# Performance work log

Measured on AMD Instinct MI355X. Metric: run time of the kernel, lower is better.

Reference implementation:

```python
import jax, jax.numpy as jnp
import numpy as np

D_TOK = 64
HID = 128


def _init_linear(key, fan_in, fan_out, bias_fill=None):
    kw, kb = jax.random.split(key)
    bound = 1.0 / np.sqrt(fan_in)
    W = jax.random.uniform(kw, (fan_in, fan_out), jnp.float32, -bound, bound)
    if bias_fill is None:
        b = jax.random.uniform(kb, (fan_out,), jnp.float32, -bound, bound)
    else:
        b = jnp.full((fan_out,), bias_fill, jnp.float32)
    return W, b


def setup_inputs() -> dict:
    key = jax.random.key(0)
    ks = jax.random.split(key, 7)
    N, E = 20000, 16
    tokens = jax.random.normal(ks[0], (N, E, D_TOK), jnp.float32)
    enc_W1, enc_b1 = _init_linear(ks[1], D_TOK, HID)
    enc_W2, enc_b2 = _init_linear(ks[2], HID, HID)
    spec_W1, spec_b1 = _init_linear(ks[3], 4 * HID, HID)
    spec_W2, spec_b2 = _init_linear(ks[4], HID, 1)
    def_W1, def_b1 = _init_linear(ks[5], 3 * HID, HID)
    def_W2, def_b2 = _init_linear(ks[6], HID, 1, bias_fill=-1.0)  # config.defer_bias
    return {
        "tokens": tokens,
        "enc_W1": enc_W1, "enc_b1": enc_b1, "enc_W2": enc_W2, "enc_b2": enc_b2,
        "spec_W1": spec_W1, "spec_b1": spec_b1, "spec_W2": spec_W2, "spec_b2": spec_b2,
        "def_W1": def_W1, "def_b1": def_b1, "def_W2": def_W2, "def_b2": def_b2,
        "full_index": 0,
        "top_k": 2,
    }


def _apply_top_k_mask(logits, full_index, top_k):
    # logits: [N, E]; mimic torch _apply_top_k_mask
    N, E = logits.shape
    if E <= 1:
        return logits
    neg = jnp.finfo(logits.dtype).min
    k = max(1, min(int(top_k), E - 1))
    masked = logits.at[:, full_index].set(neg)
    _, idx = jax.lax.top_k(masked, k)  # [N, k]
    rows = jnp.arange(N)[:, None]
    keep = jnp.zeros((N, E), bool).at[rows, idx].set(True)
    keep = keep.at[:, full_index].set(False)
    return jnp.where(keep, masked, neg)


def reference(tokens, enc_W1, enc_b1, enc_W2, enc_b2,
              spec_W1, spec_b1, spec_W2, spec_b2,
              def_W1, def_b1, def_W2, def_b2,
              full_index, top_k):
    neg = jnp.finfo(tokens.dtype).min
    # token encoder: two Linear+ReLU, applied per (row, expert)
    h = jax.nn.relu(tokens @ enc_W1 + enc_b1)
    encoded = jax.nn.relu(h @ enc_W2 + enc_b2)          # [N, E, H]
    full_token = encoded[:, full_index:full_index + 1]  # [N, 1, H]
    global_token = encoded.mean(axis=1, keepdims=True)  # [N, 1, H]
    token_delta = encoded - full_token
    global_delta = encoded - global_token
    pair = jnp.concatenate([encoded, token_delta, global_delta,
                            jnp.abs(token_delta)], axis=-1)  # [N, E, 4H]
    spec_h = jax.nn.relu(pair @ spec_W1 + spec_b1)
    specialist_logits = (spec_h @ spec_W2 + spec_b2)[..., 0]  # [N, E]
    specialist_logits = specialist_logits.at[:, full_index].set(neg)
    sparse_logits = _apply_top_k_mask(specialist_logits, full_index, top_k)
    w = jax.nn.softmax(sparse_logits, axis=1)
    w = w.at[:, full_index].set(0.0)
    mass = w.sum(axis=1, keepdims=True)
    w = jnp.where(mass > 0, w / jnp.maximum(mass, 1e-8), jnp.zeros_like(w))
    pooled = jnp.concatenate([full_token[:, 0], global_token[:, 0],
                              jnp.abs(token_delta).mean(axis=1)], axis=1)  # [N, 3H]
    def_h = jax.nn.relu(pooled @ def_W1 + def_b1)
    defer_prob = jax.nn.sigmoid(def_h @ def_W2 + def_b2)  # [N, 1]
    return w, defer_prob
```

## Files before the change

### kernel.cpp

```cpp
#include <hip/hip_runtime.h>
#include <math.h>

#define E 16
#define D 64
#define H 128
#define R 4
#define ROWS (R * E)
#define MW 16

__global__ void wabc_prep(const float* __restrict__ specW1, float* __restrict__ wabc) {
    int i = blockIdx.x * blockDim.x + threadIdx.x;
    if (i < H * H) {
        wabc[i] = specW1[i] + specW1[H * H + i] + specW1[2 * H * H + i];
    }
}

__device__ inline float waveReduceSum(float v) {
#pragma unroll
    for (int off = 32; off; off >>= 1) v += __shfl_xor(v, off, 64);
    return v;
}

template <bool USE_WABC>
__global__ __launch_bounds__(256, 2)
void router_kernel(const float* __restrict__ tokens,
                   const float* __restrict__ encW1, const float* __restrict__ encB1,
                   const float* __restrict__ encW2, const float* __restrict__ encB2,
                   const float* __restrict__ specW1, const float* __restrict__ specB1,
                   const float* __restrict__ specW2,
                   const float* __restrict__ defW1, const float* __restrict__ defB1,
                   const float* __restrict__ defW2, const float* __restrict__ defB2,
                   const int* __restrict__ fiPtr, const int* __restrict__ tkPtr,
                   const float* __restrict__ wabc,
                   float* __restrict__ out, int N) {
    __shared__ float bufA[ROWS * H];
    __shared__ float bufB[ROWS * H];
    __shared__ float s_glob[R * H];
    __shared__ float s_mabs[R * H];
    __shared__ float s_bias[R * H];
    __shared__ float s_pB[2 * R * H];
    __shared__ float s_pD[2 * R * H];
    __shared__ float s_logits[ROWS];
    __shared__ float s_dred[R];

    const int tid   = threadIdx.x;
    const int n0    = blockIdx.x * R;
    const int fi    = fiPtr[0];
    const int lane  = tid & 63;
    const int wq    = tid >> 6;
    const int j0    = lane * 2;
    const int mbase = wq * MW;

    {
        const size_t base  = (size_t)n0 * (E * D);
        const size_t total = (size_t)N * (E * D);
        float4* dst = (float4*)bufA;
#pragma unroll
        for (int it = 0; it < 4; it++) {
            int f = tid + it * 256;
            size_t off = base + (size_t)f * 4;
            float4 v = make_float4(0.f, 0.f, 0.f, 0.f);
            if (off + 3 < total) v = *(const float4*)(tokens + off);
            dst[f] = v;
        }
    }
    __syncthreads();

    {
        float acc[MW][2];
#pragma unroll
        for (int m = 0; m < MW; m++) { acc[m][0] = 0.f; acc[m][1] = 0.f; }
#pragma unroll 2
        for (int k = 0; k < D; k += 4) {
            float2 w0 = *(const float2*)(encW1 + (k + 0) * H + j0);
            float2 w1 = *(const float2*)(encW1 + (k + 1) * H + j0);
            float2 w2 = *(const float2*)(encW1 + (k + 2) * H + j0);
            float2 w3 = *(const float2*)(encW1 + (k + 3) * H + j0);
#pragma unroll
            for (int m = 0; m < MW; m++) {
                float4 t = *(const float4*)(bufA + (mbase + m) * D + k);
                acc[m][0] = fmaf(t.w, w3.x, fmaf(t.z, w2.x, fmaf(t.y, w1.x, fmaf(t.x, w0.x, acc[m][0]))));
                acc[m][1] = fmaf(t.w, w3.y, fmaf(t.z, w2.y, fmaf(t.y, w1.y, fmaf(t.x, w0.y, acc[m][1]))));
            }
        }
        float2 b = *(const float2*)(encB1 + j0);
#pragma unroll
        for (int m = 0; m < MW; m++) {
            float2 o;
            o.x = fmaxf(acc[m][0] + b.x, 0.f);
            o.y = fmaxf(acc[m][1] + b.y, 0.f);
            *(float2*)(bufB + (mbase + m) * H + j0) = o;
        }
    }
    __syncthreads();

    {
        float acc[MW][2];
#pragma unroll
        for (int m = 0; m < MW; m++) { acc[m][0] = 0.f; acc[m][1] = 0.f; }
#pragma unroll 2
        for (int k = 0; k < H; k += 4) {
            float2 w0 = *(const float2*)(encW2 + (k + 0) * H + j0);
            float2 w1 = *(const float2*)(encW2 + (k + 1) * H + j0);
            float2 w2 = *(const float2*)(encW2 + (k + 2) * H + j0);
            float2 w3 = *(const float2*)(encW2 + (k + 3) * H + j0);
#pragma unroll
            for (int m = 0; m < MW; m++) {
                float4 t = *(const float4*)(bufB + (mbase + m) * H + k);
                acc[m][0] = fmaf(t.w, w3.x, fmaf(t.z, w2.x, fmaf(t.y, w1.x, fmaf(t.x, w0.x, acc[m][0]))));
                acc[m][1] = fmaf(t.w, w3.y, fmaf(t.z, w2.y, fmaf(t.y, w1.y, fmaf(t.x, w0.y, acc[m][1]))));
            }
        }
        float2 b = *(const float2*)(encB2 + j0);
#pragma unroll
        for (int m = 0; m < MW; m++) {
            float2 o;
            o.x = fmaxf(acc[m][0] + b.x, 0.f);
            o.y = fmaxf(acc[m][1] + b.y, 0.f);
            *(float2*)(bufA + (mbase + m) * H + j0) = o;
        }
    }
    __syncthreads();

    {
        const int r4 = tid >> 6;
        const int cb = tid & 63;
#pragma unroll
        for (int half = 0; half < 2; half++) {
            const int c = cb + half * 64;
            const float* er = bufA + (r4 * E) * H + c;
            float s = 0.f;
#pragma unroll
            for (int e = 0; e < E; e++) s += er[e * H];
            float g  = s * (1.f / 16.f);
            float fc = er[fi * H];
            float ma = 0.f;
#pragma unroll
            for (int e = 0; e < E; e++) {
                float d = er[e * H] - fc;
                float a = fabsf(d);
                bufB[(r4 * E + e) * H + c] = a;
                ma += a;
            }
            s_glob[r4 * H + c] = g;
            s_mabs[r4 * H + c] = ma * (1.f / 16.f);
        }
    }
    __syncthreads();

    {
        const int jp = tid & 63;
        const int jj = jp * 2;
        const int kh = (tid >> 6) & 1;
        const int rg = tid >> 7;
        const int c0 = kh * 64;
        const float* Wb = specW1 + H * H;
        const float* Wc = specW1 + 2 * H * H;
        float accB[2][2] = {{0.f, 0.f}, {0.f, 0.f}};
        float accD[2][2] = {{0.f, 0.f}, {0.f, 0.f}};
        for (int cc = 0; cc < 64; cc++) {
            const int c = c0 + cc;
            float2 wb = *(const float2*)(Wb + c * H + jj);
            float2 wc = *(const float2*)(Wc + c * H + jj);
            float2 d0 = *(const float2*)(defW1 + c * H + jj);
            float2 d1 = *(const float2*)(defW1 + (H + c) * H + jj);
            float2 d2 = *(const float2*)(defW1 + (2 * H + c) * H + jj);
#pragma unroll
            for (int rl = 0; rl < 2; rl++) {
                const int r = rg * 2 + rl;
                float fv = bufA[(r * E + fi) * H + c];
                float gv = s_glob[r * H + c];
                float mv = s_mabs[r * H + c];
                accB[rl][0] = fmaf(fv, wb.x, accB[rl][0]);
                accB[rl][1] = fmaf(fv, wb.y, accB[rl][1]);
                accB[rl][0] = fmaf(gv, wc.x, accB[rl][0]);
                accB[rl][1] = fmaf(gv, wc.y, accB[rl][1]);
                accD[rl][0] = fmaf(fv, d0.x, accD[rl][0]);
                accD[rl][1] = fmaf(fv, d0.y, accD[rl][1]);
                accD[rl][0] = fmaf(gv, d1.x, accD[rl][0]);
                accD[rl][1] = fmaf(gv, d1.y, accD[rl][1]);
                accD[rl][0] = fmaf(mv, d2.x, accD[rl][0]);
                accD[rl][1] = fmaf(mv, d2.y, accD[rl][1]);
            }
        }
#pragma unroll
        for (int rl = 0; rl < 2; rl++) {
            const int r = rg * 2 + rl;
            *(float2*)(s_pB + (kh * R + r) * H + jj) = make_float2(accB[rl][0], accB[rl][1]);
            *(float2*)(s_pD + (kh * R + r) * H + jj) = make_float2(accD[rl][0], accD[rl][1]);
        }
    }
    __syncthreads();

    {
        float dv = 0.f;
#pragma unroll
        for (int t = 0; t < 2; t++) {
            const int j = lane + t * 64;
            float pb = s_pB[wq * H + j] + s_pB[(R + wq) * H + j];
            s_bias[wq * H + j] = specB1[j] - pb;
            float pd = defB1[j] + s_pD[wq * H + j] + s_pD[(R + wq) * H + j];
            dv += fmaxf(pd, 0.f) * defW2[j];
        }
        dv = waveReduceSum(dv);
        if (lane == 0) s_dred[wq] = dv;
    }
    __syncthreads();

    {
        float acc[MW][2];
#pragma unroll
        for (int m = 0; m < MW; m++) { acc[m][0] = 0.f; acc[m][1] = 0.f; }
        for (int c = 0; c < H; c += 4) {
            float2 wa0, wa1, wa2, wa3;
            if (USE_WABC) {
                wa0 = *(const float2*)(wabc + (c + 0) * H + j0);
                wa1 = *(const float2*)(wabc + (c + 1) * H + j0);
                wa2 = *(const float2*)(wabc + (c + 2) * H + j0);
                wa3 = *(const float2*)(wabc + (c + 3) * H + j0);
            } else {
#pragma unroll
                for (int t = 0; t < 4; t++) {
                    float2 a0 = *(const float2*)(specW1 + (c + t) * H + j0);
                    float2 a1 = *(const float2*)(specW1 + (H + c + t) * H + j0);
                    float2 a2 = *(const float2*)(specW1 + (2 * H + c + t) * H + j0);
                    float2 s2; s2.x = a0.x + a1.x + a2.x; s2.y = a0.y + a1.y + a2.y;
                    if (t == 0) wa0 = s2; else if (t == 1) wa1 = s2; else if (t == 2) wa2 = s2; else wa3 = s2;
                }
            }
            float2 wd0 = *(const float2*)(specW1 + (3 * H + c + 0) * H + j0);
            float2 wd1 = *(const float2*)(specW1 + (3 * H + c + 1) * H + j0);
            float2 wd2 = *(const float2*)(specW1 + (3 * H + c + 2) * H + j0);
            float2 wd3 = *(const float2*)(specW1 + (3 * H + c + 3) * H + j0);
#pragma unroll
            for (int m = 0; m < MW; m++) {
                float4 ev = *(const float4*)(bufA + (mbase + m) * H + c);
                float4 av = *(const float4*)(bufB + (mbase + m) * H + c);
                float a0 = acc[m][0], a1 = acc[m][1];
                a0 = fmaf(ev.x, wa0.x, a0); a0 = fmaf(ev.y, wa1.x, a0);
                a0 = fmaf(ev.z, wa2.x, a0); a0 = fmaf(ev.w, wa3.x, a0);
                a0 = fmaf(av.x, wd0.x, a0); a0 = fmaf(av.y, wd1.x, a0);
                a0 = fmaf(av.z, wd2.x, a0); a0 = fmaf(av.w, wd3.x, a0);
                a1 = fmaf(ev.x, wa0.y, a1); a1 = fmaf(ev.y, wa1.y, a1);
                a1 = fmaf(ev.z, wa2.y, a1); a1 = fmaf(ev.w, wa3.y, a1);
                a1 = fmaf(av.x, wd0.y, a1); a1 = fmaf(av.y, wd1.y, a1);
                a1 = fmaf(av.z, wd2.y, a1); a1 = fmaf(av.w, wd3.y, a1);
                acc[m][0] = a0; acc[m][1] = a1;
            }
        }
        float2 bn = *(const float2*)(s_bias + wq * H + j0);
        float2 w2 = *(const float2*)(specW2 + j0);
#pragma unroll
        for (int m = 0; m < MW; m++) {
            float h0 = fmaxf(acc[m][0] + bn.x, 0.f);
            float h1 = fmaxf(acc[m][1] + bn.y, 0.f);
            float p  = h0 * w2.x + h1 * w2.y;
            p = waveReduceSum(p);
            if (lane == 0) s_logits[mbase + m] = p;
        }
    }
    __syncthreads();

    if (tid < R && (n0 + tid) < N) {
        const int r = tid;
        const int n = n0 + r;
        float s = s_dred[r] + defB2[0];
        out[(size_t)N * E + n] = 1.f / (1.f + expf(-s));
        int k = tkPtr[0];
        if (k < 1) k = 1;
        if (k > E - 1) k = E - 1;
        unsigned chosen = 0u;
        for (int kk = 0; kk < k; kk++) {
            float bv = -INFINITY;
            int bi = 0;
            for (int e = 0; e < E; e++) {
                if (e == fi || ((chosen >> e) & 1u)) continue;
                float v = s_logits[r * E + e];
                if (v > bv) { bv = v; bi = e; }
            }
            chosen |= (1u << bi);
        }
        float mx = -INFINITY;
        for (int e = 0; e < E; e++)
            if ((chosen >> e) & 1u) { float v = s_logits[r * E + e]; if (v > mx) mx = v; }
        float ssum = 0.f;
        for (int e = 0; e < E; e++)
            if ((chosen >> e) & 1u) ssum += expf(s_logits[r * E + e] - mx);
        float inv = 1.f / ssum;
        for (int e = 0; e < E; e++) {
            float wv = 0.f;
            if ((chosen >> e) & 1u) wv = expf(s_logits[r * E + e] - mx) * inv;
            out[(size_t)n * E + e] = wv;
        }
    }
}

extern "C" void kernel_launch(void* const* d_in, const int* in_sizes, int n_in,
                              void* d_out, int out_size, void* d_ws, size_t ws_size,
                              hipStream_t stream) {
    (void)n_in; (void)out_size;
    const float* tokens = (const float*)d_in[0];
    const float* encW1  = (const float*)d_in[1];
    const float* encB1  = (const float*)d_in[2];
    const float* encW2  = (const float*)d_in[3];
    const float* encB2  = (const float*)d_in[4];
    const float* specW1 = (const float*)d_in[5];
    const float* specB1 = (const float*)d_in[6];
    const float* specW2 = (const float*)d_in[7];
    const float* defW1  = (const float*)d_in[9];
    const float* defB1  = (const float*)d_in[10];
    const float* defW2  = (const float*)d_in[11];
    const float* defB2  = (const float*)d_in[12];
    const int*   fiPtr  = (const int*)d_in[13];
    const int*   tkPtr  = (const int*)d_in[14];
    float* out = (float*)d_out;

    const int N = in_sizes[0] / (E * D);
    const int grid = (N + R - 1) / R;
    const bool useWs = (d_ws != nullptr) && (ws_size >= (size_t)(H * H * sizeof(float)));

    if (useWs) {
        wabc_prep<<<(H * H + 255) / 256, 256, 0, stream>>>(specW1, (float*)d_ws);
        router_kernel<true><<<grid, 256, 0, stream>>>(
            tokens, encW1, encB1, encW2, encB2, specW1, specB1, specW2,
            defW1, defB1, defW2, defB2, fiPtr, tkPtr, (const float*)d_ws, out, N);
    } else {
        router_kernel<false><<<grid, 256, 0, stream>>>(
            tokens, encW1, encB1, encW2, encB2, specW1, specB1, specW2,
            defW1, defB1, defW2, defB2, fiPtr, tkPtr, nullptr, out, N);
    }
}
```

Measured before the change: 761.2 us.

## Remap GEMMs so each lane owns a token row and waves own output-column slices

Restructures all three per-token GEMMs so each lane computes one (row, expert) token and each wave computes a 32-column slice. Weights are read as wave-uniform (scalar) loads and tokens are read straight from global memory, with no LDS staging. The |token_delta| buffer is no longer stored; it is recomputed on the fly from the encoded values and the full token, and LDS rows are padded to avoid bank conflicts. Specialist logits become per-wave partial sums that are added in the final top-k stage. This removes the cross-lane wave reductions, but each thread now holds 32 accumulators, and the uncoalesced per-row token loads may hurt.

```diff
diff --git a/kernel.cpp b/kernel.cpp
--- a/kernel.cpp
+++ b/kernel.cpp
@@ -6,19 +6,13 @@
 #define H 128
 #define R 4
 #define ROWS (R * E)
-#define MW 16
+#define PAD 130
 
 __global__ void wabc_prep(const float* __restrict__ specW1, float* __restrict__ wabc) {
     int i = blockIdx.x * blockDim.x + threadIdx.x;
     if (i < H * H) {
         wabc[i] = specW1[i] + specW1[H * H + i] + specW1[2 * H * H + i];
     }
-}
-
-__device__ inline float waveReduceSum(float v) {
-#pragma unroll
-    for (int off = 32; off; off >>= 1) v += __shfl_xor(v, off, 64);
-    return v;
 }
 
 template <bool USE_WABC>
@@ -33,129 +27,111 @@
                    const int* __restrict__ fiPtr, const int* __restrict__ tkPtr,
                    const float* __restrict__ wabc,
                    float* __restrict__ out, int N) {
-    __shared__ float bufA[ROWS * H];
-    __shared__ float bufB[ROWS * H];
+    __shared__ float bufH[ROWS * PAD];
+    __shared__ float bufE[ROWS * PAD];
+    __shared__ float s_full[R * H];
     __shared__ float s_glob[R * H];
     __shared__ float s_mabs[R * H];
     __shared__ float s_bias[R * H];
-    __shared__ float s_pB[2 * R * H];
-    __shared__ float s_pD[2 * R * H];
-    __shared__ float s_logits[ROWS];
+    __shared__ float s_lp[4 * ROWS];
     __shared__ float s_dred[R];
 
-    const int tid   = threadIdx.x;
-    const int n0    = blockIdx.x * R;
-    const int fi    = fiPtr[0];
-    const int lane  = tid & 63;
-    const int wq    = tid >> 6;
-    const int j0    = lane * 2;
-    const int mbase = wq * MW;
-
-    {
-        const size_t base  = (size_t)n0 * (E * D);
-        const size_t total = (size_t)N * (E * D);
-        float4* dst = (float4*)bufA;
-#pragma unroll
-        for (int it = 0; it < 4; it++) {
-            int f = tid + it * 256;
-            size_t off = base + (size_t)f * 4;
-            float4 v = make_float4(0.f, 0.f, 0.f, 0.f);
-            if (off + 3 < total) v = *(const float4*)(tokens + off);
-            dst[f] = v;
-        }
-    }
-    __syncthreads();
-
-    {
-        float acc[MW][2];
-#pragma unroll
-        for (int m = 0; m < MW; m++) { acc[m][0] = 0.f; acc[m][1] = 0.f; }
-#pragma unroll 2
-        for (int k = 0; k < D; k += 4) {
-            float2 w0 = *(const float2*)(encW1 + (k + 0) * H + j0);
-            float2 w1 = *(const float2*)(encW1 + (k + 1) * H + j0);
-            float2 w2 = *(const float2*)(encW1 + (k + 2) * H + j0);
-            float2 w3 = *(const float2*)(encW1 + (k + 3) * H + j0);
-#pragma unroll
-            for (int m = 0; m < MW; m++) {
-                float4 t = *(const float4*)(bufA + (mbase + m) * D + k);
-                acc[m][0] = fmaf(t.w, w3.x, fmaf(t.z, w2.x, fmaf(t.y, w1.x, fmaf(t.x, w0.x, acc[m][0]))));
-                acc[m][1] = fmaf(t.w, w3.y, fmaf(t.z, w2.y, fmaf(t.y, w1.y, fmaf(t.x, w0.y, acc[m][1]))));
-            }
-        }
-        float2 b = *(const float2*)(encB1 + j0);
-#pragma unroll
-        for (int m = 0; m < MW; m++) {
+    const int tid  = threadIdx.x;
+    const int lane = tid & 63;
+    const int wq   = tid >> 6;
+    const int jb   = __builtin_amdgcn_readfirstlane(wq) * 32;
+    const int n0   = blockIdx.x * R;
+    const int fi   = fiPtr[0];
+    const int l    = lane;
+
+    int tokRow = n0 * E + l;
+    if (tokRow >= N * E) tokRow = 0;
+    const float* tokRowPtr = tokens + (size_t)tokRow * D;
+
+    float acc[32];
+
+#pragma unroll
+    for (int j = 0; j < 32; j++) acc[j] = 0.f;
+    for (int k = 0; k < D; k += 2) {
+        float2 a2 = *(const float2*)(tokRowPtr + k);
+        const float* __restrict__ w0 = encW1 + k * H + jb;
+        const float* __restrict__ w1 = encW1 + (k + 1) * H + jb;
+#pragma unroll
+        for (int j = 0; j < 32; j++) {
+            acc[j] = fmaf(a2.x, w0[j], acc[j]);
+            acc[j] = fmaf(a2.y, w1[j], acc[j]);
+        }
+    }
+    {
+        const float* __restrict__ b = encB1 + jb;
+#pragma unroll
+        for (int t = 0; t < 16; t++) {
             float2 o;
-            o.x = fmaxf(acc[m][0] + b.x, 0.f);
-            o.y = fmaxf(acc[m][1] + b.y, 0.f);
-            *(float2*)(bufB + (mbase + m) * H + j0) = o;
-        }
-    }
-    __syncthreads();
-
-    {
-        float acc[MW][2];
-#pragma unroll
-        for (int m = 0; m < MW; m++) { acc[m][0] = 0.f; acc[m][1] = 0.f; }
-#pragma unroll 2
-        for (int k = 0; k < H; k += 4) {
-            float2 w0 = *(const float2*)(encW2 + (k + 0) * H + j0);
-            float2 w1 = *(const float2*)(encW2 + (k + 1) * H + j0);
-            float2 w2 = *(const float2*)(encW2 + (k + 2) * H + j0);
-            float2 w3 = *(const float2*)(encW2 + (k + 3) * H + j0);
-#pragma unroll
-            for (int m = 0; m < MW; m++) {
-                float4 t = *(const float4*)(bufB + (mbase + m) * H + k);
-                acc[m][0] = fmaf(t.w, w3.x, fmaf(t.z, w2.x, fmaf(t.y, w1.x, fmaf(t.x, w0.x, acc[m][0]))));
-                acc[m][1] = fmaf(t.w, w3.y, fmaf(t.z, w2.y, fmaf(t.y, w1.y, fmaf(t.x, w0.y, acc[m][1]))));
-            }
-        }
-        float2 b = *(const float2*)(encB2 + j0);
-#pragma unroll
-        for (int m = 0; m < MW; m++) {
+            o.x = fmaxf(acc[2 * t] + b[2 * t], 0.f);
+            o.y = fmaxf(acc[2 * t + 1] + b[2 * t + 1], 0.f);
+            *(float2*)(bufH + l * PAD + jb + 2 * t) = o;
+        }
+    }
+    __syncthreads();
+
+#pragma unroll
+    for (int j = 0; j < 32; j++) acc[j] = 0.f;
+    for (int k = 0; k < H; k += 2) {
+        float2 a2 = *(const float2*)(bufH + l * PAD + k);
+        const float* __restrict__ w0 = encW2 + k * H + jb;
+        const float* __restrict__ w1 = encW2 + (k + 1) * H + jb;
+#pragma unroll
+        for (int j = 0; j < 32; j++) {
+            acc[j] = fmaf(a2.x, w0[j], acc[j]);
+            acc[j] = fmaf(a2.y, w1[j], acc[j]);
+        }
+    }
+    {
+        const float* __restrict__ b = encB2 + jb;
+#pragma unroll
+        for (int t = 0; t < 16; t++) {
             float2 o;
-            o.x = fmaxf(acc[m][0] + b.x, 0.f);
-            o.y = fmaxf(acc[m][1] + b.y, 0.f);
-            *(float2*)(bufA + (mbase + m) * H + j0) = o;
-        }
-    }
-    __syncthreads();
-
-    {
-        const int r4 = tid >> 6;
+            o.x = fmaxf(acc[2 * t] + b[2 * t], 0.f);
+            o.y = fmaxf(acc[2 * t + 1] + b[2 * t + 1], 0.f);
+            *(float2*)(bufE + l * PAD + jb + 2 * t) = o;
+        }
+    }
+    __syncthreads();
+
+    {
+        const int r  = tid >> 6;
         const int cb = tid & 63;
 #pragma unroll
         for (int half = 0; half < 2; half++) {
             const int c = cb + half * 64;
-            const float* er = bufA + (r4 * E) * H + c;
+            const float* er = bufE + (r * E) * PAD + c;
+            float v[E];
+#pragma unroll
+            for (int e = 0; e < E; e++) v[e] = er[e * PAD];
             float s = 0.f;
 #pragma unroll
-            for (int e = 0; e < E; e++) s += er[e * H];
-            float g  = s * (1.f / 16.f);
-            float fc = er[fi * H];
+            for (int e = 0; e < E; e++) s += v[e];
+            float fc = v[fi];
             float ma = 0.f;
 #pragma unroll
-            for (int e = 0; e < E; e++) {
-                float d = er[e * H] - fc;
-                float a = fabsf(d);
-                bufB[(r4 * E + e) * H + c] = a;
-                ma += a;
-            }
-            s_glob[r4 * H + c] = g;
-            s_mabs[r4 * H + c] = ma * (1.f / 16.f);
-        }
-    }
-    __syncthreads();
-
+            for (int e = 0; e < E; e++) ma += fabsf(v[e] - fc);
+            s_full[r * H + c] = fc;
+            s_glob[r * H + c] = s * (1.f / 16.f);
+            s_mabs[r * H + c] = ma * (1.f / 16.f);
+        }
+    }
+    __syncthreads();
+
+    float* s_pB = bufH;
+    float* s_pD = bufH + 2 * R * H;
     {
         const int jp = tid & 63;
         const int jj = jp * 2;
         const int kh = (tid >> 6) & 1;
         const int rg = tid >> 7;
         const int c0 = kh * 64;
-        const float* Wb = specW1 + H * H;
-        const float* Wc = specW1 + 2 * H * H;
+        const float* __restrict__ Wb = specW1 + H * H;
+        const float* __restrict__ Wc = specW1 + 2 * H * H;
         float accB[2][2] = {{0.f, 0.f}, {0.f, 0.f}};
         float accD[2][2] = {{0.f, 0.f}, {0.f, 0.f}};
         for (int cc = 0; cc < 64; cc++) {
@@ -168,7 +144,7 @@
 #pragma unroll
             for (int rl = 0; rl < 2; rl++) {
                 const int r = rg * 2 + rl;
-                float fv = bufA[(r * E + fi) * H + c];
+                float fv = s_full[r * H + c];
                 float gv = s_glob[r * H + c];
                 float mv = s_mabs[r * H + c];
                 accB[rl][0] = fmaf(fv, wb.x, accB[rl][0]);
@@ -202,62 +178,56 @@
             float pd = defB1[j] + s_pD[wq * H + j] + s_pD[(R + wq) * H + j];
             dv += fmaxf(pd, 0.f) * defW2[j];
         }
-        dv = waveReduceSum(dv);
+#pragma unroll
+        for (int off = 32; off; off >>= 1) dv += __shfl_xor(dv, off, 64);
         if (lane == 0) s_dred[wq] = dv;
     }
     __syncthreads();
 
-    {
-        float acc[MW][2];
-#pragma unroll
-        for (int m = 0; m < MW; m++) { acc[m][0] = 0.f; acc[m][1] = 0.f; }
-        for (int c = 0; c < H; c += 4) {
-            float2 wa0, wa1, wa2, wa3;
+#pragma unroll
+    for (int j = 0; j < 32; j++) acc[j] = 0.f;
+    {
+        const int rr = l >> 4;
+        const float* __restrict__ Wd = specW1 + 3 * H * H;
+        for (int k = 0; k < H; k += 2) {
+            float2 e2 = *(const float2*)(bufE + l * PAD + k);
+            float2 f2 = *(const float2*)(s_full + rr * H + k);
+            float a0 = fabsf(e2.x - f2.x);
+            float a1 = fabsf(e2.y - f2.y);
+            const float* __restrict__ wd0 = Wd + k * H + jb;
+            const float* __restrict__ wd1 = Wd + (k + 1) * H + jb;
             if (USE_WABC) {
-                wa0 = *(const float2*)(wabc + (c + 0) * H + j0);
-                wa1 = *(const float2*)(wabc + (c + 1) * H + j0);
-                wa2 = *(const float2*)(wabc + (c + 2) * H + j0);
-                wa3 = *(const float2*)(wabc + (c + 3) * H + j0);
+                const float* __restrict__ wa0 = wabc + k * H + jb;
+                const float* __restrict__ wa1 = wabc + (k + 1) * H + jb;
+#pragma unroll
+                for (int j = 0; j < 32; j++) {
+                    acc[j] = fmaf(e2.x, wa0[j], acc[j]);
+                    acc[j] = fmaf(e2.y, wa1[j], acc[j]);
+                    acc[j] = fmaf(a0, wd0[j], acc[j]);
+                    acc[j] = fmaf(a1, wd1[j], acc[j]);
+                }
             } else {
-#pragma unroll
-                for (int t = 0; t < 4; t++) {
-                    float2 a0 = *(const float2*)(specW1 + (c + t) * H + j0);
-                    float2 a1 = *(const float2*)(specW1 + (H + c + t) * H + j0);
-                    float2 a2 = *(const float2*)(specW1 + (2 * H + c + t) * H + j0);
-                    float2 s2; s2.x = a0.x + a1.x + a2.x; s2.y = a0.y + a1.y + a2.y;
-                    if (t == 0) wa0 = s2; else if (t == 1) wa1 = s2; else if (t == 2) wa2 = s2; else wa3 = s2;
+                const float* __restrict__ p0 = specW1 + k * H + jb;
+                const float* __restrict__ p1 = specW1 + (k + 1) * H + jb;
+#pragma unroll
+                for (int j = 0; j < 32; j++) {
+                    float w_a0 = p0[j] + p0[H * H + j] + p0[2 * H * H + j];
+                    float w_a1 = p1[j] + p1[H * H + j] + p1[2 * H * H + j];
+                    acc[j] = fmaf(e2.x, w_a0, acc[j]);
+                    acc[j] = fmaf(e2.y, w_a1, acc[j]);
+                    acc[j] = fmaf(a0, wd0[j], acc[j]);
+                    acc[j] = fmaf(a1, wd1[j], acc[j]);
                 }
             }
-            float2 wd0 = *(const float2*)(specW1 + (3 * H + c + 0) * H + j0);
-            float2 wd1 = *(const float2*)(specW1 + (3 * H + c + 1) * H + j0);
-            float2 wd2 = *(const float2*)(specW1 + (3 * H + c + 2) * H + j0);
-            float2 wd3 = *(const float2*)(specW1 + (3 * H + c + 3) * H + j0);
-#pragma unroll
-            for (int m = 0; m < MW; m++) {
-                float4 ev = *(const float4*)(bufA + (mbase + m) * H + c);
-                float4 av = *(const float4*)(bufB + (mbase + m) * H + c);
-                float a0 = acc[m][0], a1 = acc[m][1];
-                a0 = fmaf(ev.x, wa0.x, a0); a0 = fmaf(ev.y, wa1.x, a0);
-                a0 = fmaf(ev.z, wa2.x, a0); a0 = fmaf(ev.w, wa3.x, a0);
-                a0 = fmaf(av.x, wd0.x, a0); a0 = fmaf(av.y, wd1.x, a0);
-                a0 = fmaf(av.z, wd2.x, a0); a0 = fmaf(av.w, wd3.x, a0);
-                a1 = fmaf(ev.x, wa0.y, a1); a1 = fmaf(ev.y, wa1.y, a1);
-                a1 = fmaf(ev.z, wa2.y, a1); a1 = fmaf(ev.w, wa3.y, a1);
-                a1 = fmaf(av.x, wd0.y, a1); a1 = fmaf(av.y, wd1.y, a1);
-                a1 = fmaf(av.z, wd2.y, a1); a1 = fmaf(av.w, wd3.y, a1);
-                acc[m][0] = a0; acc[m][1] = a1;
-            }
-        }
-        float2 bn = *(const float2*)(s_bias + wq * H + j0);
-        float2 w2 = *(const float2*)(specW2 + j0);
-#pragma unroll
-        for (int m = 0; m < MW; m++) {
-            float h0 = fmaxf(acc[m][0] + bn.x, 0.f);
-            float h1 = fmaxf(acc[m][1] + bn.y, 0.f);
-            float p  = h0 * w2.x + h1 * w2.y;
-            p = waveReduceSum(p);
-            if (lane == 0) s_logits[mbase + m] = p;
-        }
+        }
+        float p = 0.f;
+        const float* __restrict__ w2 = specW2 + jb;
+#pragma unroll
+        for (int j = 0; j < 32; j++) {
+            float b = s_bias[rr * H + jb + j];
+            p += fmaxf(acc[j] + b, 0.f) * w2[j];
+        }
+        s_lp[wq * ROWS + l] = p;
     }
     __syncthreads();
 
@@ -266,6 +236,11 @@
         const int n = n0 + r;
         float s = s_dred[r] + defB2[0];
         out[(size_t)N * E + n] = 1.f / (1.f + expf(-s));
+        float lg[E];
+#pragma unroll
+        for (int e = 0; e < E; e++)
+            lg[e] = s_lp[0 * ROWS + r * E + e] + s_lp[1 * ROWS + r * E + e]
+                  + s_lp[2 * ROWS + r * E + e] + s_lp[3 * ROWS + r * E + e];
         int k = tkPtr[0];
         if (k < 1) k = 1;
         if (k > E - 1) k = E - 1;
@@ -275,21 +250,21 @@
             int bi = 0;
             for (int e = 0; e < E; e++) {
                 if (e == fi || ((chosen >> e) & 1u)) continue;
-                float v = s_logits[r * E + e];
+                float v = lg[e];
                 if (v > bv) { bv = v; bi = e; }
             }
             chosen |= (1u << bi);
         }
         float mx = -INFINITY;
         for (int e = 0; e < E; e++)
-            if ((chosen >> e) & 1u) { float v = s_logits[r * E + e]; if (v > mx) mx = v; }
+            if ((chosen >> e) & 1u) { float v = lg[e]; if (v > mx) mx = v; }
         float ssum = 0.f;
         for (int e = 0; e < E; e++)
-            if ((chosen >> e) & 1u) ssum += expf(s_logits[r * E + e] - mx);
+            if ((chosen >> e) & 1u) ssum += expf(lg[e] - mx);
         float inv = 1.f / ssum;
         for (int e = 0; e < E; e++) {
             float wv = 0.f;
-            if ((chosen >> e) & 1u) wv = expf(s_logits[r * E + e] - mx) * inv;
+            if ((chosen >> e) & 1u) wv = expf(lg[e] - mx) * inv;
             out[(size_t)n * E + e] = wv;
         }
     }
```

Result: slower. 943.3 us (+23.9%).

## Retile GEMMs to 8x4 register tiles and recompute abs-delta on the fly

Applied to the files above, without the earlier changes.

Each wave's GEMM stages switch from 16 rows by 2 columns per lane to 8 rows by 4 columns, split across two half-waves. This halves the LDS activation reads per FMA and uses float4 weight loads. The abs(token_delta) tensor is no longer written to shared memory; it is recomputed from the encoded values and a new per-row full-token buffer inside the specialist GEMM. The freed buffer is reused for the partial sums, which lowers LDS footprint. The logits reduction now runs over 32-lane half-waves, and register pressure changes with the larger column tile.

```diff
diff --git a/kernel.cpp b/kernel.cpp
--- a/kernel.cpp
+++ b/kernel.cpp
@@ -13,12 +13,6 @@
     if (i < H * H) {
         wabc[i] = specW1[i] + specW1[H * H + i] + specW1[2 * H * H + i];
     }
-}
-
-__device__ inline float waveReduceSum(float v) {
-#pragma unroll
-    for (int off = 32; off; off >>= 1) v += __shfl_xor(v, off, 64);
-    return v;
 }
 
 template <bool USE_WABC>
@@ -35,11 +29,10 @@
                    float* __restrict__ out, int N) {
     __shared__ float bufA[ROWS * H];
     __shared__ float bufB[ROWS * H];
+    __shared__ float s_full[R * H];
     __shared__ float s_glob[R * H];
     __shared__ float s_mabs[R * H];
     __shared__ float s_bias[R * H];
-    __shared__ float s_pB[2 * R * H];
-    __shared__ float s_pD[2 * R * H];
     __shared__ float s_logits[ROWS];
     __shared__ float s_dred[R];
 
@@ -48,8 +41,11 @@
     const int fi    = fiPtr[0];
     const int lane  = tid & 63;
     const int wq    = tid >> 6;
-    const int j0    = lane * 2;
     const int mbase = wq * MW;
+    const int hw    = lane >> 5;
+    const int jl    = lane & 31;
+    const int jw0   = jl * 4;
+    const int mb2   = mbase + hw * 8;
 
     {
         const size_t base  = (size_t)n0 * (E * D);
@@ -67,57 +63,69 @@
     __syncthreads();
 
     {
-        float acc[MW][2];
-#pragma unroll
-        for (int m = 0; m < MW; m++) { acc[m][0] = 0.f; acc[m][1] = 0.f; }
+        float acc[8][4];
+#pragma unroll
+        for (int m = 0; m < 8; m++)
+#pragma unroll
+            for (int j = 0; j < 4; j++) acc[m][j] = 0.f;
 #pragma unroll 2
         for (int k = 0; k < D; k += 4) {
-            float2 w0 = *(const float2*)(encW1 + (k + 0) * H + j0);
-            float2 w1 = *(const float2*)(encW1 + (k + 1) * H + j0);
-            float2 w2 = *(const float2*)(encW1 + (k + 2) * H + j0);
-            float2 w3 = *(const float2*)(encW1 + (k + 3) * H + j0);
-#pragma unroll
-            for (int m = 0; m < MW; m++) {
-                float4 t = *(const float4*)(bufA + (mbase + m) * D + k);
+            float4 w0 = *(const float4*)(encW1 + (k + 0) * H + jw0);
+            float4 w1 = *(const float4*)(encW1 + (k + 1) * H + jw0);
+            float4 w2 = *(const float4*)(encW1 + (k + 2) * H + jw0);
+            float4 w3 = *(const float4*)(encW1 + (k + 3) * H + jw0);
+#pragma unroll
+            for (int m = 0; m < 8; m++) {
+                float4 t = *(const float4*)(bufA + (mb2 + m) * D + k);
                 acc[m][0] = fmaf(t.w, w3.x, fmaf(t.z, w2.x, fmaf(t.y, w1.x, fmaf(t.x, w0.x, acc[m][0]))));
                 acc[m][1] = fmaf(t.w, w3.y, fmaf(t.z, w2.y, fmaf(t.y, w1.y, fmaf(t.x, w0.y, acc[m][1]))));
-            }
-        }
-        float2 b = *(const float2*)(encB1 + j0);
-#pragma unroll
-        for (int m = 0; m < MW; m++) {
-            float2 o;
+                acc[m][2] = fmaf(t.w, w3.z, fmaf(t.z, w2.z, fmaf(t.y, w1.z, fmaf(t.x, w0.z, acc[m][2]))));
+                acc[m][3] = fmaf(t.w, w3.w, fmaf(t.z, w2.w, fmaf(t.y, w1.w, fmaf(t.x, w0.w, acc[m][3]))));
+            }
+        }
+        float4 b = *(const float4*)(encB1 + jw0);
+#pragma unroll
+        for (int m = 0; m < 8; m++) {
+            float4 o;
             o.x = fmaxf(acc[m][0] + b.x, 0.f);
             o.y = fmaxf(acc[m][1] + b.y, 0.f);
-            *(float2*)(bufB + (mbase + m) * H + j0) = o;
-        }
-    }
-    __syncthreads();
-
-    {
-        float acc[MW][2];
-#pragma unroll
-        for (int m = 0; m < MW; m++) { acc[m][0] = 0.f; acc[m][1] = 0.f; }
+            o.z = fmaxf(acc[m][2] + b.z, 0.f);
+            o.w = fmaxf(acc[m][3] + b.w, 0.f);
+            *(float4*)(bufB + (mb2 + m) * H + jw0) = o;
+        }
+    }
+    __syncthreads();
+
+    {
+        float acc[8][4];
+#pragma unroll
+        for (int m = 0; m < 8; m++)
+#pragma unroll
+            for (int j = 0; j < 4; j++) acc[m][j] = 0.f;
 #pragma unroll 2
         for (int k = 0; k < H; k += 4) {
-            float2 w0 = *(const float2*)(encW2 + (k + 0) * H + j0);
-            float2 w1 = *(const float2*)(encW2 + (k + 1) * H + j0);
-            float2 w2 = *(const float2*)(encW2 + (k + 2) * H + j0);
-            float2 w3 = *(const float2*)(encW2 + (k + 3) * H + j0);
-#pragma unroll
-            for (int m = 0; m < MW; m++) {
-                float4 t = *(const float4*)(bufB + (mbase + m) * H + k);
+            float4 w0 = *(const float4*)(encW2 + (k + 0) * H + jw0);
+            float4 w1 = *(const float4*)(encW2 + (k + 1) * H + jw0);
+            float4 w2 = *(const float4*)(encW2 + (k + 2) * H + jw0);
+            float4 w3 = *(const float4*)(encW2 + (k + 3) * H + jw0);
+#pragma unroll
+            for (int m = 0; m < 8; m++) {
+                float4 t = *(const float4*)(bufB + (mb2 + m) * H + k);
                 acc[m][0] = fmaf(t.w, w3.x, fmaf(t.z, w2.x, fmaf(t.y, w1.x, fmaf(t.x, w0.x, acc[m][0]))));
                 acc[m][1] = fmaf(t.w, w3.y, fmaf(t.z, w2.y, fmaf(t.y, w1.y, fmaf(t.x, w0.y, acc[m][1]))));
-            }
-        }
-        float2 b = *(const float2*)(encB2 + j0);
-#pragma unroll
-        for (int m = 0; m < MW; m++) {
-            float2 o;
+                acc[m][2] = fmaf(t.w, w3.z, fmaf(t.z, w2.z, fmaf(t.y, w1.z, fmaf(t.x, w0.z, acc[m][2]))));
+                acc[m][3] = fmaf(t.w, w3.w, fmaf(t.z, w2.w, fmaf(t.y, w1.w, fmaf(t.x, w0.w, acc[m][3]))));
+            }
+        }
+        float4 b = *(const float4*)(encB2 + jw0);
+#pragma unroll
+        for (int m = 0; m < 8; m++) {
+            float4 o;
             o.x = fmaxf(acc[m][0] + b.x, 0.f);
             o.y = fmaxf(acc[m][1] + b.y, 0.f);
-            *(float2*)(bufA + (mbase + m) * H + j0) = o;
+            o.z = fmaxf(acc[m][2] + b.z, 0.f);
+            o.w = fmaxf(acc[m][3] + b.w, 0.f);
+            *(float4*)(bufA + (mb2 + m) * H + jw0) = o;
         }
     }
     __syncthreads();
@@ -129,33 +137,33 @@
         for (int half = 0; half < 2; half++) {
             const int c = cb + half * 64;
             const float* er = bufA + (r4 * E) * H + c;
+            float v[E];
+#pragma unroll
+            for (int e = 0; e < E; e++) v[e] = er[e * H];
             float s = 0.f;
 #pragma unroll
-            for (int e = 0; e < E; e++) s += er[e * H];
-            float g  = s * (1.f / 16.f);
-            float fc = er[fi * H];
+            for (int e = 0; e < E; e++) s += v[e];
+            float fc = v[fi];
             float ma = 0.f;
 #pragma unroll
-            for (int e = 0; e < E; e++) {
-                float d = er[e * H] - fc;
-                float a = fabsf(d);
-                bufB[(r4 * E + e) * H + c] = a;
-                ma += a;
-            }
-            s_glob[r4 * H + c] = g;
+            for (int e = 0; e < E; e++) ma += fabsf(v[e] - fc);
+            s_full[r4 * H + c] = fc;
+            s_glob[r4 * H + c] = s * (1.f / 16.f);
             s_mabs[r4 * H + c] = ma * (1.f / 16.f);
         }
     }
     __syncthreads();
 
+    float* s_pB = bufB;
+    float* s_pD = bufB + 2 * R * H;
     {
         const int jp = tid & 63;
         const int jj = jp * 2;
         const int kh = (tid >> 6) & 1;
         const int rg = tid >> 7;
         const int c0 = kh * 64;
-        const float* Wb = specW1 + H * H;
-        const float* Wc = specW1 + 2 * H * H;
+        const float* __restrict__ Wb = specW1 + H * H;
+        const float* __restrict__ Wc = specW1 + 2 * H * H;
         float accB[2][2] = {{0.f, 0.f}, {0.f, 0.f}};
         float accD[2][2] = {{0.f, 0.f}, {0.f, 0.f}};
         for (int cc = 0; cc < 64; cc++) {
@@ -168,7 +176,7 @@
 #pragma unroll
             for (int rl = 0; rl < 2; rl++) {
                 const int r = rg * 2 + rl;
-                float fv = bufA[(r * E + fi) * H + c];
+                float fv = s_full[r * H + c];
                 float gv = s_glob[r * H + c];
                 float mv = s_mabs[r * H + c];
                 accB[rl][0] = fmaf(fv, wb.x, accB[rl][0]);
@@ -202,61 +210,80 @@
             float pd = defB1[j] + s_pD[wq * H + j] + s_pD[(R + wq) * H + j];
             dv += fmaxf(pd, 0.f) * defW2[j];
         }
-        dv = waveReduceSum(dv);
+#pragma unroll
+        for (int off = 32; off; off >>= 1) dv += __shfl_xor(dv, off, 64);
         if (lane == 0) s_dred[wq] = dv;
     }
     __syncthreads();
 
     {
-        float acc[MW][2];
-#pragma unroll
-        for (int m = 0; m < MW; m++) { acc[m][0] = 0.f; acc[m][1] = 0.f; }
-        for (int c = 0; c < H; c += 4) {
-            float2 wa0, wa1, wa2, wa3;
+        float acc[8][4];
+#pragma unroll
+        for (int m = 0; m < 8; m++)
+#pragma unroll
+            for (int j = 0; j < 4; j++) acc[m][j] = 0.f;
+        const float* __restrict__ Wd = specW1 + 3 * H * H;
+        for (int k = 0; k < H; k += 4) {
+            float4 wa0, wa1, wa2, wa3;
             if (USE_WABC) {
-                wa0 = *(const float2*)(wabc + (c + 0) * H + j0);
-                wa1 = *(const float2*)(wabc + (c + 1) * H + j0);
-                wa2 = *(const float2*)(wabc + (c + 2) * H + j0);
-                wa3 = *(const float2*)(wabc + (c + 3) * H + j0);
+                wa0 = *(const float4*)(wabc + (k + 0) * H + jw0);
+                wa1 = *(const float4*)(wabc + (k + 1) * H + jw0);
+                wa2 = *(const float4*)(wabc + (k + 2) * H + jw0);
+                wa3 = *(const float4*)(wabc + (k + 3) * H + jw0);
             } else {
 #pragma unroll
                 for (int t = 0; t < 4; t++) {
-                    float2 a0 = *(const float2*)(specW1 + (c + t) * H + j0);
-                    float2 a1 = *(const float2*)(specW1 + (H + c + t) * H + j0);
-                    float2 a2 = *(const float2*)(specW1 + (2 * H + c + t) * H + j0);
-                    float2 s2; s2.x = a0.x + a1.x + a2.x; s2.y = a0.y + a1.y + a2.y;
-                    if (t == 0) wa0 = s2; else if (t == 1) wa1 = s2; else if (t == 2) wa2 = s2; else wa3 = s2;
+                    const float* p = specW1 + (k + t) * H + jw0;
+                    float4 x0 = *(const float4*)(p);
+                    float4 x1 = *(const float4*)(p + H * H);
+                    float4 x2 = *(const float4*)(p + 2 * H * H);
+                    float4 s4 = make_float4(x0.x + x1.x + x2.x, x0.y + x1.y + x2.y,
+                                            x0.z + x1.z + x2.z, x0.w + x1.w + x2.w);
+                    if (t == 0) wa0 = s4; else if (t == 1) wa1 = s4;
+                    else if (t == 2) wa2 = s4; else wa3 = s4;
                 }
             }
-            float2 wd0 = *(const float2*)(specW1 + (3 * H + c + 0) * H + j0);
-            float2 wd1 = *(const float2*)(specW1 + (3 * H + c + 1) * H + j0);
-            float2 wd2 = *(const float2*)(specW1 + (3 * H + c + 2) * H + j0);
-            float2 wd3 = *(const float2*)(specW1 + (3 * H + c + 3) * H + j0);
-#pragma unroll
-            for (int m = 0; m < MW; m++) {
-                float4 ev = *(const float4*)(bufA + (mbase + m) * H + c);
-                float4 av = *(const float4*)(bufB + (mbase + m) * H + c);
-                float a0 = acc[m][0], a1 = acc[m][1];
-                a0 = fmaf(ev.x, wa0.x, a0); a0 = fmaf(ev.y, wa1.x, a0);
-                a0 = fmaf(ev.z, wa2.x, a0); a0 = fmaf(ev.w, wa3.x, a0);
-                a0 = fmaf(av.x, wd0.x, a0); a0 = fmaf(av.y, wd1.x, a0);
-                a0 = fmaf(av.z, wd2.x, a0); a0 = fmaf(av.w, wd3.x, a0);
-                a1 = fmaf(ev.x, wa0.y, a1); a1 = fmaf(ev.y, wa1.y, a1);
-                a1 = fmaf(ev.z, wa2.y, a1); a1 = fmaf(ev.w, wa3.y, a1);
-                a1 = fmaf(av.x, wd0.y, a1); a1 = fmaf(av.y, wd1.y, a1);
-                a1 = fmaf(av.z, wd2.y, a1); a1 = fmaf(av.w, wd3.y, a1);
-                acc[m][0] = a0; acc[m][1] = a1;
-            }
-        }
-        float2 bn = *(const float2*)(s_bias + wq * H + j0);
-        float2 w2 = *(const float2*)(specW2 + j0);
-#pragma unroll
-        for (int m = 0; m < MW; m++) {
-            float h0 = fmaxf(acc[m][0] + bn.x, 0.f);
-            float h1 = fmaxf(acc[m][1] + bn.y, 0.f);
-            float p  = h0 * w2.x + h1 * w2.y;
-            p = waveReduceSum(p);
-            if (lane == 0) s_logits[mbase + m] = p;
+            float4 wd0 = *(const float4*)(Wd + (k + 0) * H + jw0);
+            float4 wd1 = *(const float4*)(Wd + (k + 1) * H + jw0);
+            float4 wd2 = *(const float4*)(Wd + (k + 2) * H + jw0);
+            float4 wd3 = *(const float4*)(Wd + (k + 3) * H + jw0);
+            float4 f4 = *(const float4*)(s_full + wq * H + k);
+#pragma unroll
+            for (int m = 0; m < 8; m++) {
+                float4 ev = *(const float4*)(bufA + (mb2 + m) * H + k);
+                float ax = fabsf(ev.x - f4.x);
+                float ay = fabsf(ev.y - f4.y);
+                float az = fabsf(ev.z - f4.z);
+                float aw = fabsf(ev.w - f4.w);
+#pragma unroll
+                for (int j = 0; j < 4; j++) {
+                    const float* waj0 = &wa0.x, *waj1 = &wa1.x, *waj2 = &wa2.x, *waj3 = &wa3.x;
+                    const float* wdj0 = &wd0.x, *wdj1 = &wd1.x, *wdj2 = &wd2.x, *wdj3 = &wd3.x;
+                    float a = acc[m][j];
+                    a = fmaf(ev.x, waj0[j], a);
+                    a = fmaf(ev.y, waj1[j], a);
+                    a = fmaf(ev.z, waj2[j], a);
+                    a = fmaf(ev.w, waj3[j], a);
+                    a = fmaf(ax, wdj0[j], a);
+                    a = fmaf(ay, wdj1[j], a);
+                    a = fmaf(az, wdj2[j], a);
+                    a = fmaf(aw, wdj3[j], a);
+                    acc[m][j] = a;
+                }
+            }
+        }
+        float4 bn = *(const float4*)(s_bias + wq * H + jw0);
+        float4 w2 = *(const float4*)(specW2 + jw0);
+#pragma unroll
+        for (int m = 0; m < 8; m++) {
+            float p = 0.f;
+            p += fmaxf(acc[m][0] + bn.x, 0.f) * w2.x;
+            p += fmaxf(acc[m][1] + bn.y, 0.f) * w2.y;
+            p += fmaxf(acc[m][2] + bn.z, 0.f) * w2.z;
+            p += fmaxf(acc[m][3] + bn.w, 0.f) * w2.w;
+#pragma unroll
+            for (int off = 1; off < 32; off <<= 1) p += __shfl_xor(p, off, 64);
+            if (jl == 0) s_logits[mb2 + m] = p;
         }
     }
     __syncthreads();
```

New measurement: 739.5 us. -2.9%, faster.
